# Optimization experiments

Measured on AMD Instinct MI355X. Metric: run time of the kernel, lower is better.

The kernel has to match this reference:

```python
import jax, jax.numpy as jnp
import numpy as np

N_NODES = 50000
N_EDGES = 800000
IN_DIM, HID_DIM, OUT_DIM, N_CLASSES = 128, 256, 64, 40


def _xavier(key, shape):
    fan_in, fan_out = shape[0], shape[1]
    std = float(np.sqrt(2.0 / (fan_in + fan_out)))
    return jax.random.normal(key, shape, dtype=jnp.float32) * std


def gcn_conv(x, W, b, src, dst, n_nodes):
    """PyG GCNConv: add self-loops, symmetric D^-1/2 (A+I) D^-1/2 X W + b."""
    h = x @ W  # [N, out]
    loop = jnp.arange(n_nodes, dtype=src.dtype)
    s = jnp.concatenate([src, loop])  # sources (messages flow src -> dst)
    d = jnp.concatenate([dst, loop])
    ones = jnp.ones(s.shape[0], dtype=h.dtype)
    deg = jax.ops.segment_sum(ones, d, num_segments=n_nodes)  # in-degree incl. self-loop
    dinv = jnp.where(deg > 0, jax.lax.rsqrt(deg), 0.0)
    norm = dinv[s] * dinv[d]  # [E+N]
    msg = h[s] * norm[:, None]
    out = jax.ops.segment_sum(msg, d, num_segments=n_nodes)
    return out + b


def setup_inputs() -> dict:
    key = jax.random.key(0)
    ks = jax.random.split(key, 9)
    x = jax.random.normal(ks[0], (N_NODES, IN_DIM), dtype=jnp.float32)
    edge_index = jax.random.randint(ks[1], (2, N_EDGES), 0, N_NODES, dtype=jnp.int64)
    return {
        "x": x,
        "edge_index": edge_index,
        "W1": _xavier(ks[2], (IN_DIM, HID_DIM)),
        "b1": jnp.zeros((HID_DIM,), jnp.float32),
        "W2": _xavier(ks[3], (HID_DIM, OUT_DIM)),
        "b2": jnp.zeros((OUT_DIM,), jnp.float32),
        "Wp1": _xavier(ks[4], (2 * OUT_DIM, 4 * OUT_DIM)),
        "bp1": jnp.zeros((4 * OUT_DIM,), jnp.float32),
        "Wp2": _xavier(ks[5], (4 * OUT_DIM, OUT_DIM)),
        "bp2": jnp.zeros((OUT_DIM,), jnp.float32),
        "Wc": _xavier(ks[6], (OUT_DIM, N_CLASSES)),
        "bc": jnp.zeros((N_CLASSES,), jnp.float32),
    }


def reference(x, edge_index, W1, b1, W2, b2, Wp1, bp1, Wp2, bp2, Wc, bc):
    src, dst = edge_index[0], edge_index[1]
    n = x.shape[0]
    h = jax.nn.relu(gcn_conv(x, W1, b1, src, dst, n))  # [N, HID]
    f = gcn_conv(h, W2, b2, src, dst, n)  # [N, OUT]
    # edge MLP on gathered endpoint features
    ef = jnp.concatenate([f[src], f[dst]], axis=-1)  # [E, 2*OUT]
    ef = jax.nn.relu(ef @ Wp1 + bp1)  # [E, 4*OUT]
    edge_feats = ef @ Wp2 + bp2  # [E, OUT]
    logits = f @ Wc + bc  # [N, C]
    return f, edge_feats, logits, edge_index
```

## Files before the change

### kernel.cpp

```cpp
#include <hip/hip_runtime.h>

#define N_NODES   50000
#define N_EDGES   800000
#define IN_DIM    128
#define HID_DIM   256
#define OUT_DIM   64
#define N_CLASSES 40

typedef __attribute__((ext_vector_type(8))) short short8;
typedef __attribute__((ext_vector_type(8))) unsigned short ushort8;
typedef __attribute__((ext_vector_type(4))) float f32x4;

__device__ inline short f2bf(float x) {
    unsigned u = __builtin_bit_cast(unsigned, x);
    unsigned r = (u + 0x7FFFu + ((u >> 16) & 1u)) >> 16;
    return (short)r;
}
__device__ inline float bf2f(unsigned short u) {
    unsigned v = ((unsigned)u) << 16;
    return __builtin_bit_cast(float, v);
}
__device__ __host__ inline int swap23(int p) {
    return (p & 0xC3) | ((p >> 2) & 0x0C) | ((p << 2) & 0x30);
}


__global__ void k_prep(const float* __restrict__ x,
                       const float* __restrict__ W1, const float* __restrict__ W2,
                       const float* __restrict__ Wp1, const float* __restrict__ Wp2,
                       unsigned short* __restrict__ xb,
                       short* __restrict__ W1t, short* __restrict__ W2t,
                       short* __restrict__ Wp1t, short* __restrict__ Wp2t,
                       int* __restrict__ degi, int* __restrict__ cursor) {
    int i = blockIdx.x * 256 + threadIdx.x;
    if (i < N_NODES) { degi[i] = 0; cursor[i] = 0; }
    if (i < 128 * 256) {
        int k = i >> 8, n = i & 255;
        W1t[n * 128 + k]  = f2bf(W1[i]);
        Wp1t[n * 128 + k] = f2bf(Wp1[i]);
    }
    if (i < 256 * 64) {
        int p = i >> 6, o = i & 63;
        int h = swap23(p);
        W2t[o * 256 + p]  = f2bf(W2[h * 64 + o]);
        Wp2t[o * 256 + p] = f2bf(Wp2[h * 64 + o]);
    }
    if (i < N_NODES * IN_DIM / 4) {
        float4 v = ((const float4*)x)[i];
        ushort4 u;
        u.x = (unsigned short)f2bf(v.x); u.y = (unsigned short)f2bf(v.y);
        u.z = (unsigned short)f2bf(v.z); u.w = (unsigned short)f2bf(v.w);
        ((ushort4*)xb)[i] = u;
    }
}


__global__ void k_deg_count(const int* __restrict__ dst, int* __restrict__ degi) {
    int e = blockIdx.x * 256 + threadIdx.x;
    if (e < N_EDGES) atomicAdd(&degi[dst[e]], 1);
}

__global__ void k_scan_bsum(const int* __restrict__ vals, int n, int* __restrict__ bsum,
                            float* __restrict__ dinv) {
    __shared__ int sm[256];
    int t = threadIdx.x, i = blockIdx.x * 256 + t;
    int d = (i < n) ? vals[i] : 0;
    if (i < n) dinv[i] = rsqrtf((float)(d + 1));
    sm[t] = d;
    __syncthreads();
    for (int s = 128; s > 0; s >>= 1) {
        if (t < s) sm[t] += sm[t + s];
        __syncthreads();
    }
    if (t == 0) bsum[blockIdx.x] = sm[0];
}

__global__ void k_scan_bscan(int* __restrict__ bsum, int nb) {
    __shared__ int sm[256];
    int t = threadIdx.x;
    int orig = (t < nb) ? bsum[t] : 0;
    sm[t] = orig;
    __syncthreads();
    for (int off = 1; off < 256; off <<= 1) {
        int v = (t >= off) ? sm[t - off] : 0;
        __syncthreads();
        sm[t] += v;
        __syncthreads();
    }
    if (t < nb) bsum[t] = sm[t] - orig;
}

__global__ void k_scan_final(const int* __restrict__ vals, int n,
                             const int* __restrict__ bscan, int* __restrict__ out) {
    __shared__ int sm[256];
    int t = threadIdx.x, i = blockIdx.x * 256 + t;
    int orig = (i < n) ? vals[i] : 0;
    sm[t] = orig;
    __syncthreads();
    for (int off = 1; off < 256; off <<= 1) {
        int v = (t >= off) ? sm[t - off] : 0;
        __syncthreads();
        sm[t] += v;
        __syncthreads();
    }
    int excl = sm[t] - orig + bscan[blockIdx.x];
    if (i < n) out[i] = excl;
    if (i == n - 1) out[n] = excl + orig;
}

__global__ void k_csr_fill(const int* __restrict__ src, const int* __restrict__ dst,
                           const int* __restrict__ csr_off, int* __restrict__ cursor,
                           int* __restrict__ csr_src) {
    int e = blockIdx.x * 256 + threadIdx.x;
    if (e < N_EDGES) {
        int d = dst[e];
        int pos = csr_off[d] + atomicAdd(&cursor[d], 1);
        csr_src[pos] = src[e];
    }
}

__global__ void k_copy_ei(const int* __restrict__ ei, float* __restrict__ out) {
    int j = blockIdx.x * 256 + threadIdx.x;
    if (j < (2 * N_EDGES) / 4) {
        int4 v = ((const int4*)ei)[j];
        float4 o = {(float)v.x, (float)v.y, (float)v.z, (float)v.w};
        ((float4*)out)[j] = o;
    }
}


__global__ __launch_bounds__(256) void k_agg0(const unsigned short* __restrict__ xb,
                                              const float* __restrict__ dinv,
                                              const int* __restrict__ csr_off,
                                              const int* __restrict__ csr_src,
                                              unsigned short* __restrict__ xa) {
    const int v = blockIdx.x * 4 + (threadIdx.x >> 6);
    const int lane = threadIdx.x & 63;
    float dv = dinv[v];
    unsigned c = *(const unsigned*)(xb + (size_t)v * 128 + lane * 2);
    float a0 = bf2f((unsigned short)(c & 0xFFFF)) * dv;
    float a1 = bf2f((unsigned short)(c >> 16)) * dv;
    int beg = csr_off[v], end = csr_off[v + 1];
    for (int base = beg; base < end; base += 64) {
        int idx = base + lane;
        int sj = (idx < end) ? csr_src[idx] : 0;
        float dj = (idx < end) ? dinv[sj] : 0.f;
        int m = min(64, end - base);
        int j = 0;
        for (; j + 4 <= m; j += 4) {
            int s0 = __shfl(sj, j), s1 = __shfl(sj, j + 1);
            int s2 = __shfl(sj, j + 2), s3 = __shfl(sj, j + 3);
            float d0 = __shfl(dj, j), d1 = __shfl(dj, j + 1);
            float d2 = __shfl(dj, j + 2), d3 = __shfl(dj, j + 3);
            unsigned h0 = *(const unsigned*)(xb + (size_t)s0 * 128 + lane * 2);
            unsigned h1 = *(const unsigned*)(xb + (size_t)s1 * 128 + lane * 2);
            unsigned h2 = *(const unsigned*)(xb + (size_t)s2 * 128 + lane * 2);
            unsigned h3 = *(const unsigned*)(xb + (size_t)s3 * 128 + lane * 2);
            a0 += bf2f((unsigned short)(h0 & 0xFFFF)) * d0 + bf2f((unsigned short)(h1 & 0xFFFF)) * d1
                + bf2f((unsigned short)(h2 & 0xFFFF)) * d2 + bf2f((unsigned short)(h3 & 0xFFFF)) * d3;
            a1 += bf2f((unsigned short)(h0 >> 16)) * d0 + bf2f((unsigned short)(h1 >> 16)) * d1
                + bf2f((unsigned short)(h2 >> 16)) * d2 + bf2f((unsigned short)(h3 >> 16)) * d3;
        }
        for (; j < m; j++) {
            int s = __shfl(sj, j);
            float ds = __shfl(dj, j);
            unsigned hv = *(const unsigned*)(xb + (size_t)s * 128 + lane * 2);
            a0 += bf2f((unsigned short)(hv & 0xFFFF)) * ds;
            a1 += bf2f((unsigned short)(hv >> 16)) * ds;
        }
    }
    unsigned o = (unsigned)(unsigned short)f2bf(a0 * dv) |
                 ((unsigned)(unsigned short)f2bf(a1 * dv) << 16);
    *(unsigned*)(xa + (size_t)v * 128 + lane * 2) = o;
}


__global__ __launch_bounds__(256) void k_agg2(const unsigned short* __restrict__ h2b,
                                              const float* __restrict__ dinv,
                                              const int* __restrict__ csr_off,
                                              const int* __restrict__ csr_src,
                                              const float* __restrict__ b2,
                                              const float* __restrict__ Wc,
                                              const float* __restrict__ bc,
                                              float* __restrict__ f_out,
                                              unsigned short* __restrict__ fb,
                                              float* __restrict__ lg_out) {
    const int v = blockIdx.x * 4 + (threadIdx.x >> 6);
    const int lane = threadIdx.x & 63;
    float dv = dinv[v];
    float acc = bf2f(h2b[(size_t)v * 64 + lane]) * dv;
    int beg = csr_off[v], end = csr_off[v + 1];
    for (int base = beg; base < end; base += 64) {
        int idx = base + lane;
        int sj = (idx < end) ? csr_src[idx] : 0;
        float dj = (idx < end) ? dinv[sj] : 0.f;
        int m = min(64, end - base);
        int j = 0;
        for (; j + 4 <= m; j += 4) {
            int s0 = __shfl(sj, j), s1 = __shfl(sj, j + 1);
            int s2 = __shfl(sj, j + 2), s3 = __shfl(sj, j + 3);
            float d0 = __shfl(dj, j), d1 = __shfl(dj, j + 1);
            float d2 = __shfl(dj, j + 2), d3 = __shfl(dj, j + 3);
            float h0 = bf2f(h2b[(size_t)s0 * 64 + lane]);
            float h1 = bf2f(h2b[(size_t)s1 * 64 + lane]);
            float h2 = bf2f(h2b[(size_t)s2 * 64 + lane]);
            float h3 = bf2f(h2b[(size_t)s3 * 64 + lane]);
            acc += h0 * d0 + h1 * d1 + h2 * d2 + h3 * d3;
        }
        for (; j < m; j++) {
            int s = __shfl(sj, j);
            float ds = __shfl(dj, j);
            acc += bf2f(h2b[(size_t)s * 64 + lane]) * ds;
        }
    }
    float r = acc * dv + b2[lane];
    f_out[(size_t)v * 64 + lane] = r;
    fb[(size_t)v * 64 + lane] = (unsigned short)f2bf(r);
    bool act = lane < N_CLASSES;
    float lacc = act ? bc[lane] : 0.f;
    #pragma unroll
    for (int i2 = 0; i2 < 64; i2++) {
        float fi = __shfl(r, i2);
        if (act) lacc += fi * Wc[i2 * N_CLASSES + lane];
    }
    if (act) lg_out[(size_t)v * N_CLASSES + lane] = lacc;
}


__global__ __launch_bounds__(256) void k_gemm1_mfma(const unsigned short* __restrict__ xa,
                                                    const short* __restrict__ W1t,
                                                    const float* __restrict__ b1,
                                                    unsigned short* __restrict__ h1) {
    __shared__ unsigned short xs[64 * 128];
    const int t = threadIdx.x;
    const int lane = t & 63, wv = t >> 6, lr = lane & 15, lg = lane >> 4;
    const int nb = blockIdx.x * 64;

    #pragma unroll
    for (int i = 0; i < 4; i++) {
        int q = t + i * 256, row = q >> 4, seg = q & 15;
        int node = nb + row;
        ushort8 v = {0, 0, 0, 0, 0, 0, 0, 0};
        if (node < N_NODES) v = *(const ushort8*)(xa + (size_t)node * 128 + seg * 8);
        *(ushort8*)((char*)xs + ((row * 256 + seg * 16) ^ ((row & 7) << 4))) = v;
    }

    short8 A1[4][4];
    #pragma unroll
    for (int mi = 0; mi < 4; mi++)
        #pragma unroll
        for (int kt = 0; kt < 4; kt++)
            A1[mi][kt] = *(const short8*)(W1t + (size_t)(wv * 64 + mi * 16 + lr) * 128 + kt * 32 + lg * 8);
    __syncthreads();

    #pragma unroll
    for (int nj = 0; nj < 4; nj++) {
        short8 Bf[4];
        int nr = nj * 16 + lr;
        #pragma unroll
        for (int kt = 0; kt < 4; kt++)
            Bf[kt] = *(const short8*)((const char*)xs + ((nr * 256 + kt * 64 + lg * 16) ^ ((nr & 7) << 4)));
        int node = nb + nr;
        #pragma unroll
        for (int mh = 0; mh < 2; mh++) {
            f32x4 a0 = {0.f, 0.f, 0.f, 0.f}, a1 = {0.f, 0.f, 0.f, 0.f};
            #pragma unroll
            for (int kt = 0; kt < 4; kt++) {
                a0 = __builtin_amdgcn_mfma_f32_16x16x32_bf16(A1[mh * 2 + 0][kt], Bf[kt], a0, 0, 0, 0);
                a1 = __builtin_amdgcn_mfma_f32_16x16x32_bf16(A1[mh * 2 + 1][kt], Bf[kt], a1, 0, 0, 0);
            }
            if (node < N_NODES) {
                float4 b0 = *(const float4*)(b1 + wv * 64 + (mh * 2 + 0) * 16 + lg * 4);
                float4 b1v = *(const float4*)(b1 + wv * 64 + (mh * 2 + 1) * 16 + lg * 4);
                ushort8 pk;
                pk[0] = (unsigned short)f2bf(fmaxf(a0[0] + b0.x, 0.f));
                pk[1] = (unsigned short)f2bf(fmaxf(a0[1] + b0.y, 0.f));
                pk[2] = (unsigned short)f2bf(fmaxf(a0[2] + b0.z, 0.f));
                pk[3] = (unsigned short)f2bf(fmaxf(a0[3] + b0.w, 0.f));
                pk[4] = (unsigned short)f2bf(fmaxf(a1[0] + b1v.x, 0.f));
                pk[5] = (unsigned short)f2bf(fmaxf(a1[1] + b1v.y, 0.f));
                pk[6] = (unsigned short)f2bf(fmaxf(a1[2] + b1v.z, 0.f));
                pk[7] = (unsigned short)f2bf(fmaxf(a1[3] + b1v.w, 0.f));
                *(ushort8*)(h1 + (size_t)node * 256 + wv * 64 + lg * 16 + mh * 8) = pk;
            }
        }
    }
}


__global__ __launch_bounds__(256) void k_gemm2_mfma(const unsigned short* __restrict__ h1,
                                                    const short* __restrict__ W2t,
                                                    unsigned short* __restrict__ h2b) {
    __shared__ unsigned short hs[64 * 256];
    const int t = threadIdx.x;
    const int lane = t & 63, wv = t >> 6, lr = lane & 15, lg = lane >> 4;
    const int nb = blockIdx.x * 64;

    #pragma unroll
    for (int i = 0; i < 8; i++) {
        int q = t + i * 256, row = q >> 5, seg = q & 31;
        int node = nb + row;
        ushort8 v = {0, 0, 0, 0, 0, 0, 0, 0};
        if (node < N_NODES) v = *(const ushort8*)(h1 + (size_t)node * 256 + seg * 8);
        *(ushort8*)((char*)hs + ((row * 512 + seg * 16) ^ ((row & 7) << 4))) = v;
    }

    short8 A2[8];
    #pragma unroll
    for (int kt = 0; kt < 8; kt++)
        A2[kt] = *(const short8*)(W2t + (size_t)(wv * 16 + lr) * 256 + kt * 32 + lg * 8);
    __syncthreads();

    #pragma unroll
    for (int nj = 0; nj < 4; nj++) {
        short8 Bh[8];
        int nr = nj * 16 + lr;
        #pragma unroll
        for (int kt = 0; kt < 8; kt++)
            Bh[kt] = *(const short8*)((const char*)hs + ((nr * 512 + kt * 64 + lg * 16) ^ ((nr & 7) << 4)));
        int node = nb + nr;
        f32x4 acc = {0.f, 0.f, 0.f, 0.f};
        #pragma unroll
        for (int kt = 0; kt < 8; kt++)
            acc = __builtin_amdgcn_mfma_f32_16x16x32_bf16(A2[kt], Bh[kt], acc, 0, 0, 0);
        if (node < N_NODES) {
            ushort4 u;
            u.x = (unsigned short)f2bf(acc[0]); u.y = (unsigned short)f2bf(acc[1]);
            u.z = (unsigned short)f2bf(acc[2]); u.w = (unsigned short)f2bf(acc[3]);
            *(ushort4*)(h2b + (size_t)node * 64 + wv * 16 + lg * 4) = u;
        }
    }
}


__global__ __launch_bounds__(256) void k_edge_mlpC(
        const unsigned short* __restrict__ fb,
        const int* __restrict__ src, const int* __restrict__ dst,
        const short* __restrict__ Wp1t, const float* __restrict__ bp1,
        const short* __restrict__ Wp2t, const float* __restrict__ bp2,
        float* __restrict__ out, int n_tiles) {
    __shared__ unsigned short hid_s[2][32 * 256];

    const int t = threadIdx.x;
    const int lane = t & 63, wv = t >> 6, lr = lane & 15, lg = lane >> 4;

    short8 A1[4][4];
    #pragma unroll
    for (int mi = 0; mi < 4; mi++)
        #pragma unroll
        for (int kt = 0; kt < 4; kt++)
            A1[mi][kt] = *(const short8*)(Wp1t + (size_t)(wv * 64 + mi * 16 + lr) * 128 + kt * 32 + lg * 8);
    short8 A2[8];
    #pragma unroll
    for (int kt = 0; kt < 8; kt++)
        A2[kt] = *(const short8*)(Wp2t + (size_t)(wv * 16 + lr) * 256 + kt * 32 + lg * 8);
    float4 bb1[4];
    #pragma unroll
    for (int mi = 0; mi < 4; mi++)
        bb1[mi] = *(const float4*)(bp1 + wv * 64 + mi * 16 + lg * 4);
    const float4 bv2 = *(const float4*)(bp2 + wv * 16 + lg * 4);

    int tile = blockIdx.x;
    if (tile >= n_tiles) return;
    const int g = gridDim.x;

    short8 Bf[2][4];
    {
        int sC[2], dC[2];
        #pragma unroll
        for (int nj = 0; nj < 2; nj++) {
            int e = tile * 32 + nj * 16 + lr;
            sC[nj] = src[e];
            dC[nj] = dst[e];
        }
        #pragma unroll
        for (int nj = 0; nj < 2; nj++) {
            const unsigned short* srow = fb + (size_t)sC[nj] * 64;
            const unsigned short* drow = fb + (size_t)dC[nj] * 64;
            Bf[nj][0] = *(const short8*)(srow + lg * 8);
            Bf[nj][1] = *(const short8*)(srow + 32 + lg * 8);
            Bf[nj][2] = *(const short8*)(drow + lg * 8);
            Bf[nj][3] = *(const short8*)(drow + 32 + lg * 8);
        }
    }
    int sA[2], dA[2];
    {
        int tn = tile + g;
        if (tn < n_tiles) {
            #pragma unroll
            for (int nj = 0; nj < 2; nj++) {
                int e = tn * 32 + nj * 16 + lr;
                sA[nj] = src[e];
                dA[nj] = dst[e];
            }
        }
    }

    int cur = 0;
    for (; tile < n_tiles; tile += g) {
        #pragma unroll
        for (int nj = 0; nj < 2; nj++) {
            int er = nj * 16 + lr;
            #pragma unroll
            for (int mh = 0; mh < 2; mh++) {
                f32x4 a0 = {0.f, 0.f, 0.f, 0.f}, a1 = {0.f, 0.f, 0.f, 0.f};
                #pragma unroll
                for (int kt = 0; kt < 4; kt++) {
                    a0 = __builtin_amdgcn_mfma_f32_16x16x32_bf16(A1[mh * 2 + 0][kt], Bf[nj][kt], a0, 0, 0, 0);
                    a1 = __builtin_amdgcn_mfma_f32_16x16x32_bf16(A1[mh * 2 + 1][kt], Bf[nj][kt], a1, 0, 0, 0);
                }
                float4 b0 = bb1[mh * 2 + 0], b1v = bb1[mh * 2 + 1];
                ushort8 pk;
                pk[0] = (unsigned short)f2bf(fmaxf(a0[0] + b0.x, 0.f));
                pk[1] = (unsigned short)f2bf(fmaxf(a0[1] + b0.y, 0.f));
                pk[2] = (unsigned short)f2bf(fmaxf(a0[2] + b0.z, 0.f));
                pk[3] = (unsigned short)f2bf(fmaxf(a0[3] + b0.w, 0.f));
                pk[4] = (unsigned short)f2bf(fmaxf(a1[0] + b1v.x, 0.f));
                pk[5] = (unsigned short)f2bf(fmaxf(a1[1] + b1v.y, 0.f));
                pk[6] = (unsigned short)f2bf(fmaxf(a1[2] + b1v.z, 0.f));
                pk[7] = (unsigned short)f2bf(fmaxf(a1[3] + b1v.w, 0.f));
                *(ushort8*)((char*)hid_s[cur] +
                    ((er * 512 + wv * 128 + lg * 32 + mh * 16) ^ ((er & 7) << 4))) = pk;
            }
        }

        int tn = tile + g;
        if (tn < n_tiles) {
            #pragma unroll
            for (int nj = 0; nj < 2; nj++) {
                const unsigned short* srow = fb + (size_t)sA[nj] * 64;
                const unsigned short* drow = fb + (size_t)dA[nj] * 64;
                Bf[nj][0] = *(const short8*)(srow + lg * 8);
                Bf[nj][1] = *(const short8*)(srow + 32 + lg * 8);
                Bf[nj][2] = *(const short8*)(drow + lg * 8);
                Bf[nj][3] = *(const short8*)(drow + 32 + lg * 8);
            }
        }
        int tnn = tile + 2 * g;
        if (tnn < n_tiles) {
            #pragma unroll
            for (int nj = 0; nj < 2; nj++) {
                int e = tnn * 32 + nj * 16 + lr;
                sA[nj] = src[e];
                dA[nj] = dst[e];
            }
        }

        asm volatile("s_waitcnt lgkmcnt(0)" ::: "memory");
        __builtin_amdgcn_s_barrier();

        #pragma unroll
        for (int nj = 0; nj < 2; nj++) {
            short8 Bh[8];
            int er = nj * 16 + lr;
            #pragma unroll
            for (int kt = 0; kt < 8; kt++)
                Bh[kt] = *(const short8*)((const char*)hid_s[cur] +
                             ((er * 512 + kt * 64 + lg * 16) ^ ((er & 7) << 4)));
            f32x4 acc = {0.f, 0.f, 0.f, 0.f};
            #pragma unroll
            for (int kt = 0; kt < 8; kt++)
                acc = __builtin_amdgcn_mfma_f32_16x16x32_bf16(A2[kt], Bh[kt], acc, 0, 0, 0);
            float4 o = {acc[0] + bv2.x, acc[1] + bv2.y, acc[2] + bv2.z, acc[3] + bv2.w};
            *(float4*)(out + (size_t)(tile * 32 + er) * 64 + wv * 16 + lg * 4) = o;
        }
        cur ^= 1;
    }
}


extern "C" void kernel_launch(void* const* d_in, const int* in_sizes, int n_in,
                              void* d_out, int out_size, void* d_ws, size_t ws_size,
                              hipStream_t stream) {
    const float* x   = (const float*)d_in[0];
    const int*   ei  = (const int*)d_in[1];
    const float* W1  = (const float*)d_in[2];
    const float* b1  = (const float*)d_in[3];
    const float* W2  = (const float*)d_in[4];
    const float* b2  = (const float*)d_in[5];
    const float* Wp1 = (const float*)d_in[6];
    const float* bp1 = (const float*)d_in[7];
    const float* Wp2 = (const float*)d_in[8];
    const float* bp2 = (const float*)d_in[9];
    const float* Wc  = (const float*)d_in[10];
    const float* bc  = (const float*)d_in[11];

    const int* src = ei;
    const int* dst = ei + N_EDGES;

    float* out    = (float*)d_out;
    float* f_out  = out;
    float* ef_out = out + (size_t)N_NODES * OUT_DIM;
    float* lg_out = ef_out + (size_t)N_EDGES * OUT_DIM;
    float* ei_out = lg_out + (size_t)N_NODES * N_CLASSES;

    char* p = (char*)d_ws;
    auto alloc = [&](size_t bytes) -> char* {
        char* r = p;
        p += (bytes + 255) / 256 * 256;
        return r;
    };
    unsigned short* xb   = (unsigned short*)alloc((size_t)N_NODES * IN_DIM * 2);
    unsigned short* xa   = (unsigned short*)alloc((size_t)N_NODES * IN_DIM * 2);
    unsigned short* h1   = (unsigned short*)alloc((size_t)N_NODES * HID_DIM * 2);
    unsigned short* h2b  = (unsigned short*)alloc((size_t)N_NODES * OUT_DIM * 2);
    unsigned short* fb   = (unsigned short*)alloc((size_t)N_NODES * OUT_DIM * 2);
    int*   degi    = (int*)alloc((size_t)N_NODES * 4);
    float* dinv    = (float*)alloc((size_t)N_NODES * 4);
    int*   csr_off = (int*)alloc((size_t)(N_NODES + 1) * 4);
    int*   cursor  = (int*)alloc((size_t)N_NODES * 4);
    int*   csr_src = (int*)alloc((size_t)N_EDGES * 4);
    int*   bsum    = (int*)alloc(256 * 4);
    short* W1t     = (short*)alloc((size_t)256 * 128 * 2);
    short* W2t     = (short*)alloc((size_t)64 * 256 * 2);
    short* Wp1t    = (short*)alloc((size_t)256 * 128 * 2);
    short* Wp2t    = (short*)alloc((size_t)64 * 256 * 2);

    const int nbScan = (N_NODES + 255) / 256;

    k_prep<<<(N_NODES * IN_DIM / 4 + 255) / 256, 256, 0, stream>>>(
        x, W1, W2, Wp1, Wp2, xb, W1t, W2t, Wp1t, Wp2t, degi, cursor);
    k_deg_count<<<(N_EDGES + 255) / 256, 256, 0, stream>>>(dst, degi);
    k_scan_bsum<<<nbScan, 256, 0, stream>>>(degi, N_NODES, bsum, dinv);
    k_scan_bscan<<<1, 256, 0, stream>>>(bsum, nbScan);
    k_scan_final<<<nbScan, 256, 0, stream>>>(degi, N_NODES, bsum, csr_off);
    k_csr_fill<<<(N_EDGES + 255) / 256, 256, 0, stream>>>(src, dst, csr_off, cursor, csr_src);

    const int nbG = (N_NODES + 63) / 64;
    k_agg0<<<N_NODES / 4, 256, 0, stream>>>(xb, dinv, csr_off, csr_src, xa);
    k_gemm1_mfma<<<nbG, 256, 0, stream>>>(xa, W1t, b1, h1);
    k_gemm2_mfma<<<nbG, 256, 0, stream>>>(h1, W2t, h2b);
    k_agg2<<<N_NODES / 4, 256, 0, stream>>>(h2b, dinv, csr_off, csr_src, b2, Wc, bc,
                                            f_out, fb, lg_out);

    k_edge_mlpC<<<1280, 256, 0, stream>>>(fb, src, dst, Wp1t, bp1, Wp2t, bp2,
                                          ef_out, N_EDGES / 32);
    k_copy_ei<<<(2 * N_EDGES / 4 + 255) / 256, 256, 0, stream>>>(ei, ei_out);
}
```

Before: 388.8 us.

## Fuse GCN layer GEMMs through LDS, fold edge-index copy into prep, use packed bf16 converts

Merges the two per-node GEMM kernels so the ReLU hidden activations stay in shared memory instead of making a round trip through a global h1 buffer. The edge-index float conversion moves into the prep kernel, which removes one launch. Manual float-to-bf16 rounding is replaced with the v_cvt_pk_bf16_f32 instruction throughout. The fused kernel uses more LDS (48KB), which may lower occupancy, and the packed conversion relies on the hardware's rounding matching the old manual round-to-nearest-even.

```diff
diff --git a/kernel.cpp b/kernel.cpp
--- a/kernel.cpp
+++ b/kernel.cpp
@@ -20,18 +20,24 @@
     unsigned v = ((unsigned)u) << 16;
     return __builtin_bit_cast(float, v);
 }
+__device__ inline unsigned cvtpk(float lo, float hi) {
+    unsigned r;
+    asm("v_cvt_pk_bf16_f32 %0, %1, %2" : "=v"(r) : "v"(lo), "v"(hi));
+    return r;
+}
 __device__ __host__ inline int swap23(int p) {
     return (p & 0xC3) | ((p >> 2) & 0x0C) | ((p << 2) & 0x30);
 }
 
 
-__global__ void k_prep(const float* __restrict__ x,
+__global__ void k_prep(const float* __restrict__ x, const int* __restrict__ ei,
                        const float* __restrict__ W1, const float* __restrict__ W2,
                        const float* __restrict__ Wp1, const float* __restrict__ Wp2,
                        unsigned short* __restrict__ xb,
                        short* __restrict__ W1t, short* __restrict__ W2t,
                        short* __restrict__ Wp1t, short* __restrict__ Wp2t,
-                       int* __restrict__ degi, int* __restrict__ cursor) {
+                       int* __restrict__ degi, int* __restrict__ cursor,
+                       float* __restrict__ ei_out) {
     int i = blockIdx.x * 256 + threadIdx.x;
     if (i < N_NODES) { degi[i] = 0; cursor[i] = 0; }
     if (i < 128 * 256) {
@@ -47,10 +53,15 @@
     }
     if (i < N_NODES * IN_DIM / 4) {
         float4 v = ((const float4*)x)[i];
-        ushort4 u;
-        u.x = (unsigned short)f2bf(v.x); u.y = (unsigned short)f2bf(v.y);
-        u.z = (unsigned short)f2bf(v.z); u.w = (unsigned short)f2bf(v.w);
-        ((ushort4*)xb)[i] = u;
+        uint2 u;
+        u.x = cvtpk(v.x, v.y);
+        u.y = cvtpk(v.z, v.w);
+        *(uint2*)((unsigned short*)xb + (size_t)i * 4) = u;
+    }
+    if (i < (2 * N_EDGES) / 4) {
+        int4 v = ((const int4*)ei)[i];
+        float4 o = {(float)v.x, (float)v.y, (float)v.z, (float)v.w};
+        ((float4*)ei_out)[i] = o;
     }
 }
 
@@ -116,15 +127,6 @@
         int d = dst[e];
         int pos = csr_off[d] + atomicAdd(&cursor[d], 1);
         csr_src[pos] = src[e];
-    }
-}
-
-__global__ void k_copy_ei(const int* __restrict__ ei, float* __restrict__ out) {
-    int j = blockIdx.x * 256 + threadIdx.x;
-    if (j < (2 * N_EDGES) / 4) {
-        int4 v = ((const int4*)ei)[j];
-        float4 o = {(float)v.x, (float)v.y, (float)v.z, (float)v.w};
-        ((float4*)out)[j] = o;
     }
 }
 
@@ -169,9 +171,7 @@
             a1 += bf2f((unsigned short)(hv >> 16)) * ds;
         }
     }
-    unsigned o = (unsigned)(unsigned short)f2bf(a0 * dv) |
-                 ((unsigned)(unsigned short)f2bf(a1 * dv) << 16);
-    *(unsigned*)(xa + (size_t)v * 128 + lane * 2) = o;
+    *(unsigned*)(xa + (size_t)v * 128 + lane * 2) = cvtpk(a0 * dv, a1 * dv);
 }
 
 
@@ -227,11 +227,13 @@
 }
 
 
-__global__ __launch_bounds__(256) void k_gemm1_mfma(const unsigned short* __restrict__ xa,
-                                                    const short* __restrict__ W1t,
-                                                    const float* __restrict__ b1,
-                                                    unsigned short* __restrict__ h1) {
+__global__ __launch_bounds__(256) void k_gemm12(const unsigned short* __restrict__ xa,
+                                                const short* __restrict__ W1t,
+                                                const float* __restrict__ b1,
+                                                const short* __restrict__ W2t,
+                                                unsigned short* __restrict__ h2b) {
     __shared__ unsigned short xs[64 * 128];
+    __shared__ unsigned short hs[64 * 256];
     const int t = threadIdx.x;
     const int lane = t & 63, wv = t >> 6, lr = lane & 15, lg = lane >> 4;
     const int nb = blockIdx.x * 64;
@@ -251,6 +253,10 @@
         #pragma unroll
         for (int kt = 0; kt < 4; kt++)
             A1[mi][kt] = *(const short8*)(W1t + (size_t)(wv * 64 + mi * 16 + lr) * 128 + kt * 32 + lg * 8);
+    float4 bb1[4];
+    #pragma unroll
+    for (int mi = 0; mi < 4; mi++)
+        bb1[mi] = *(const float4*)(b1 + wv * 64 + mi * 16 + lg * 4);
     __syncthreads();
 
     #pragma unroll
@@ -260,7 +266,6 @@
         #pragma unroll
         for (int kt = 0; kt < 4; kt++)
             Bf[kt] = *(const short8*)((const char*)xs + ((nr * 256 + kt * 64 + lg * 16) ^ ((nr & 7) << 4)));
-        int node = nb + nr;
         #pragma unroll
         for (int mh = 0; mh < 2; mh++) {
             f32x4 a0 = {0.f, 0.f, 0.f, 0.f}, a1 = {0.f, 0.f, 0.f, 0.f};
@@ -269,47 +274,22 @@
                 a0 = __builtin_amdgcn_mfma_f32_16x16x32_bf16(A1[mh * 2 + 0][kt], Bf[kt], a0, 0, 0, 0);
                 a1 = __builtin_amdgcn_mfma_f32_16x16x32_bf16(A1[mh * 2 + 1][kt], Bf[kt], a1, 0, 0, 0);
             }
-            if (node < N_NODES) {
-                float4 b0 = *(const float4*)(b1 + wv * 64 + (mh * 2 + 0) * 16 + lg * 4);
-                float4 b1v = *(const float4*)(b1 + wv * 64 + (mh * 2 + 1) * 16 + lg * 4);
-                ushort8 pk;
-                pk[0] = (unsigned short)f2bf(fmaxf(a0[0] + b0.x, 0.f));
-                pk[1] = (unsigned short)f2bf(fmaxf(a0[1] + b0.y, 0.f));
-                pk[2] = (unsigned short)f2bf(fmaxf(a0[2] + b0.z, 0.f));
-                pk[3] = (unsigned short)f2bf(fmaxf(a0[3] + b0.w, 0.f));
-                pk[4] = (unsigned short)f2bf(fmaxf(a1[0] + b1v.x, 0.f));
-                pk[5] = (unsigned short)f2bf(fmaxf(a1[1] + b1v.y, 0.f));
-                pk[6] = (unsigned short)f2bf(fmaxf(a1[2] + b1v.z, 0.f));
-                pk[7] = (unsigned short)f2bf(fmaxf(a1[3] + b1v.w, 0.f));
-                *(ushort8*)(h1 + (size_t)node * 256 + wv * 64 + lg * 16 + mh * 8) = pk;
-            }
-        }
-    }
-}
-
-
-__global__ __launch_bounds__(256) void k_gemm2_mfma(const unsigned short* __restrict__ h1,
-                                                    const short* __restrict__ W2t,
-                                                    unsigned short* __restrict__ h2b) {
-    __shared__ unsigned short hs[64 * 256];
-    const int t = threadIdx.x;
-    const int lane = t & 63, wv = t >> 6, lr = lane & 15, lg = lane >> 4;
-    const int nb = blockIdx.x * 64;
-
-    #pragma unroll
-    for (int i = 0; i < 8; i++) {
-        int q = t + i * 256, row = q >> 5, seg = q & 31;
-        int node = nb + row;
-        ushort8 v = {0, 0, 0, 0, 0, 0, 0, 0};
-        if (node < N_NODES) v = *(const ushort8*)(h1 + (size_t)node * 256 + seg * 8);
-        *(ushort8*)((char*)hs + ((row * 512 + seg * 16) ^ ((row & 7) << 4))) = v;
+            float4 b0 = bb1[mh * 2 + 0], b1v = bb1[mh * 2 + 1];
+            uint4 pkv;
+            pkv.x = cvtpk(fmaxf(a0[0] + b0.x, 0.f),  fmaxf(a0[1] + b0.y, 0.f));
+            pkv.y = cvtpk(fmaxf(a0[2] + b0.z, 0.f),  fmaxf(a0[3] + b0.w, 0.f));
+            pkv.z = cvtpk(fmaxf(a1[0] + b1v.x, 0.f), fmaxf(a1[1] + b1v.y, 0.f));
+            pkv.w = cvtpk(fmaxf(a1[2] + b1v.z, 0.f), fmaxf(a1[3] + b1v.w, 0.f));
+            *(uint4*)((char*)hs + ((nr * 512 + wv * 128 + lg * 32 + mh * 16) ^ ((nr & 7) << 4))) = pkv;
+        }
     }
 
     short8 A2[8];
     #pragma unroll
     for (int kt = 0; kt < 8; kt++)
         A2[kt] = *(const short8*)(W2t + (size_t)(wv * 16 + lr) * 256 + kt * 32 + lg * 8);
-    __syncthreads();
+    asm volatile("s_waitcnt lgkmcnt(0)" ::: "memory");
+    __builtin_amdgcn_s_barrier();
 
     #pragma unroll
     for (int nj = 0; nj < 4; nj++) {
@@ -324,10 +304,10 @@
         for (int kt = 0; kt < 8; kt++)
             acc = __builtin_amdgcn_mfma_f32_16x16x32_bf16(A2[kt], Bh[kt], acc, 0, 0, 0);
         if (node < N_NODES) {
-            ushort4 u;
-            u.x = (unsigned short)f2bf(acc[0]); u.y = (unsigned short)f2bf(acc[1]);
-            u.z = (unsigned short)f2bf(acc[2]); u.w = (unsigned short)f2bf(acc[3]);
-            *(ushort4*)(h2b + (size_t)node * 64 + wv * 16 + lg * 4) = u;
+            uint2 u;
+            u.x = cvtpk(acc[0], acc[1]);
+            u.y = cvtpk(acc[2], acc[3]);
+            *(uint2*)(h2b + (size_t)node * 64 + wv * 16 + lg * 4) = u;
         }
     }
 }
@@ -410,17 +390,13 @@
                     a1 = __builtin_amdgcn_mfma_f32_16x16x32_bf16(A1[mh * 2 + 1][kt], Bf[nj][kt], a1, 0, 0, 0);
                 }
                 float4 b0 = bb1[mh * 2 + 0], b1v = bb1[mh * 2 + 1];
-                ushort8 pk;
-                pk[0] = (unsigned short)f2bf(fmaxf(a0[0] + b0.x, 0.f));
-                pk[1] = (unsigned short)f2bf(fmaxf(a0[1] + b0.y, 0.f));
-                pk[2] = (unsigned short)f2bf(fmaxf(a0[2] + b0.z, 0.f));
-                pk[3] = (unsigned short)f2bf(fmaxf(a0[3] + b0.w, 0.f));
-                pk[4] = (unsigned short)f2bf(fmaxf(a1[0] + b1v.x, 0.f));
-                pk[5] = (unsigned short)f2bf(fmaxf(a1[1] + b1v.y, 0.f));
-                pk[6] = (unsigned short)f2bf(fmaxf(a1[2] + b1v.z, 0.f));
-                pk[7] = (unsigned short)f2bf(fmaxf(a1[3] + b1v.w, 0.f));
-                *(ushort8*)((char*)hid_s[cur] +
-                    ((er * 512 + wv * 128 + lg * 32 + mh * 16) ^ ((er & 7) << 4))) = pk;
+                uint4 pkv;
+                pkv.x = cvtpk(fmaxf(a0[0] + b0.x, 0.f),  fmaxf(a0[1] + b0.y, 0.f));
+                pkv.y = cvtpk(fmaxf(a0[2] + b0.z, 0.f),  fmaxf(a0[3] + b0.w, 0.f));
+                pkv.z = cvtpk(fmaxf(a1[0] + b1v.x, 0.f), fmaxf(a1[1] + b1v.y, 0.f));
+                pkv.w = cvtpk(fmaxf(a1[2] + b1v.z, 0.f), fmaxf(a1[3] + b1v.w, 0.f));
+                *(uint4*)((char*)hid_s[cur] +
+                    ((er * 512 + wv * 128 + lg * 32 + mh * 16) ^ ((er & 7) << 4))) = pkv;
             }
         }
 
@@ -502,7 +478,6 @@
     };
     unsigned short* xb   = (unsigned short*)alloc((size_t)N_NODES * IN_DIM * 2);
     unsigned short* xa   = (unsigned short*)alloc((size_t)N_NODES * IN_DIM * 2);
-    unsigned short* h1   = (unsigned short*)alloc((size_t)N_NODES * HID_DIM * 2);
     unsigned short* h2b  = (unsigned short*)alloc((size_t)N_NODES * OUT_DIM * 2);
     unsigned short* fb   = (unsigned short*)alloc((size_t)N_NODES * OUT_DIM * 2);
     int*   degi    = (int*)alloc((size_t)N_NODES * 4);
@@ -519,7 +494,7 @@
     const int nbScan = (N_NODES + 255) / 256;
 
     k_prep<<<(N_NODES * IN_DIM / 4 + 255) / 256, 256, 0, stream>>>(
-        x, W1, W2, Wp1, Wp2, xb, W1t, W2t, Wp1t, Wp2t, degi, cursor);
+        x, ei, W1, W2, Wp1, Wp2, xb, W1t, W2t, Wp1t, Wp2t, degi, cursor, ei_out);
     k_deg_count<<<(N_EDGES + 255) / 256, 256, 0, stream>>>(dst, degi);
     k_scan_bsum<<<nbScan, 256, 0, stream>>>(degi, N_NODES, bsum, dinv);
     k_scan_bscan<<<1, 256, 0, stream>>>(bsum, nbScan);
@@ -528,12 +503,10 @@
 
     const int nbG = (N_NODES + 63) / 64;
     k_agg0<<<N_NODES / 4, 256, 0, stream>>>(xb, dinv, csr_off, csr_src, xa);
-    k_gemm1_mfma<<<nbG, 256, 0, stream>>>(xa, W1t, b1, h1);
-    k_gemm2_mfma<<<nbG, 256, 0, stream>>>(h1, W2t, h2b);
+    k_gemm12<<<nbG, 256, 0, stream>>>(xa, W1t, b1, W2t, h2b);
     k_agg2<<<N_NODES / 4, 256, 0, stream>>>(h2b, dinv, csr_off, csr_src, b2, Wc, bc,
                                             f_out, fb, lg_out);
 
     k_edge_mlpC<<<1280, 256, 0, stream>>>(fb, src, dst, Wp1t, bp1, Wp2t, bp2,
                                           ef_out, N_EDGES / 32);
-    k_copy_ei<<<(2 * N_EDGES / 4 + 255) / 256, 256, 0, stream>>>(ei, ei_out);
-}
+}
```

Result: faster. 372.9 us (-4.1%).
